# Kernel optimization log

Hardware: AMD Instinct MI355X
Metric: run time of the kernel (lower is better)

## Reference

```python
import jax, jax.numpy as jnp
import numpy as np

INPUT_DIM = 1024
HIDDEN_DIM = 2048
NUM_BLOCKS = 8
BLOCK_SIZE = HIDDEN_DIM // NUM_BLOCKS
BATCH = 2048


def setup_inputs() -> dict:
    key = jax.random.key(0)
    ks = jax.random.split(key, 6)
    # PyTorch GRUCell init: uniform(-1/sqrt(hidden_size), 1/sqrt(hidden_size))
    bound = 1.0 / np.sqrt(BLOCK_SIZE)
    u = lambda k, shape: jax.random.uniform(k, shape, jnp.float32, -bound, bound)
    return {
        "input": jax.random.normal(ks[0], (BATCH, INPUT_DIM), jnp.float32),
        "hidden": jax.random.normal(ks[1], (BATCH, HIDDEN_DIM), jnp.float32),
        # stacked per-block GRUCell params (block-diagonal structure)
        "W_ih": u(ks[2], (NUM_BLOCKS, 3 * BLOCK_SIZE, INPUT_DIM)),
        "W_hh": u(ks[3], (NUM_BLOCKS, 3 * BLOCK_SIZE, BLOCK_SIZE)),
        "b_ih": u(ks[4], (NUM_BLOCKS, 3 * BLOCK_SIZE)),
        "b_hh": u(ks[5], (NUM_BLOCKS, 3 * BLOCK_SIZE)),
    }


def reference(input, hidden, W_ih, W_hh, b_ih, b_hh):
    B = input.shape[0]
    nb, g3, bs = W_hh.shape  # [num_blocks, 3*block_size, block_size]
    hb = hidden.reshape(B, nb, bs)                      # [B, nb, bs]
    # input-to-gate and hidden-to-gate projections, batched over blocks
    gi = jnp.einsum("bi,ngi->bng", input, W_ih) + b_ih  # [B, nb, 3*bs]
    gh = jnp.einsum("bns,ngs->bng", hb, W_hh) + b_hh    # [B, nb, 3*bs]
    i_r, i_z, i_n = jnp.split(gi, 3, axis=-1)
    h_r, h_z, h_n = jnp.split(gh, 3, axis=-1)
    r = jax.nn.sigmoid(i_r + h_r)
    z = jax.nn.sigmoid(i_z + h_z)
    n = jnp.tanh(i_n + r * h_n)
    new_h = (1.0 - z) * n + z * hb                      # [B, nb, bs]
    return new_h.reshape(B, nb * bs)
```

## Files before the change

kernel.cpp:

```cpp
#include <hip/hip_runtime.h>
#include <hip/hip_bf16.h>
#include <type_traits>

#define AS1 __attribute__((address_space(1)))
#define AS3 __attribute__((address_space(3)))

typedef __attribute__((ext_vector_type(4))) float f32x4;
typedef __attribute__((ext_vector_type(8))) short bf16x8;

template <int V> using ic = std::integral_constant<int, V>;

static constexpr int B_   = 2048;
static constexpr int IN_  = 1024;
static constexpr int HID_ = 2048;
static constexpr int NB_  = 8;
static constexpr int BS_  = 256;
static constexpr int G3_  = 768;

__device__ __forceinline__ unsigned short f2bf(float f) {
  unsigned u = __builtin_bit_cast(unsigned, f);
  u = (u + 0x7FFFu + ((u >> 16) & 1u)) >> 16;
  return (unsigned short)u;
}

__global__ void cvt_all(const float* __restrict__ x, const float* __restrict__ h,
                        const float* __restrict__ Wih, const float* __restrict__ Whh,
                        unsigned short* __restrict__ dst) {
  constexpr int c0 = (B_ * IN_) / 4;
  constexpr int c1 = c0 + (B_ * HID_) / 4;
  constexpr int c2 = c1 + (NB_ * G3_ * IN_) / 4;
  constexpr int n4 = c2 + (NB_ * G3_ * BS_) / 4;
  int i = blockIdx.x * blockDim.x + threadIdx.x;
  int stride = gridDim.x * blockDim.x;
  for (; i < n4; i += stride) {
    float4 v;
    if (i < c0)       v = reinterpret_cast<const float4*>(x)[i];
    else if (i < c1)  v = reinterpret_cast<const float4*>(h)[i - c0];
    else if (i < c2)  v = reinterpret_cast<const float4*>(Wih)[i - c1];
    else              v = reinterpret_cast<const float4*>(Whh)[i - c2];
    ushort4 o;
    o.x = f2bf(v.x); o.y = f2bf(v.y); o.z = f2bf(v.z); o.w = f2bf(v.w);
    reinterpret_cast<ushort4*>(dst)[i] = o;
  }
}

__global__ __launch_bounds__(256, 2) void gru_mfma(
    const unsigned short* __restrict__ inb,
    const unsigned short* __restrict__ hidb,
    const unsigned short* __restrict__ wihb,
    const unsigned short* __restrict__ whhb,
    const float* __restrict__ hid_f32,
    const float* __restrict__ b_ih,
    const float* __restrict__ b_hh,
    float* __restrict__ out)
{
  __shared__ __align__(16) char lds[2][40960];

  const int t    = threadIdx.x;
  const int lane = t & 63;
  const int wid  = t >> 6;
  const int wm   = wid >> 1;
  const int wn   = wid & 1;

  const int bid = blockIdx.x;
  const int swz = (bid & 7) * 64 + (bid >> 3);
  const int mt  = swz & 15;
  const int ct  = swz >> 4;
  const int mrow0 = mt * 128;
  const int n     = ct >> 2;
  const int s0    = (ct & 3) * 64;

  int arow[4], acb[4];
#pragma unroll
  for (int p = 0; p < 4; ++p) {
    int op = p * 4096 + t * 16;
    int ol = op ^ (((op >> 7) & 7) << 4);
    arow[p] = ol >> 7; acb[p] = ol & 127;
  }
  int wrowg[6], wsl[6], wcb[6];
#pragma unroll
  for (int p = 0; p < 6; ++p) {
    int op = p * 4096 + t * 16;
    int ol = op ^ (((op >> 7) & 7) << 4);
    int wr = ol >> 7;
    wrowg[p] = wr >> 6;
    wsl[p]   = wr & 63;
    wcb[p]   = ol & 127;
  }

  f32x4 acc[4][4][2] = {};

  auto stage = [&](int buf, int t2, int from, int to) {
    const bool ph1 = t2 < 16;
    const int ks = ph1 ? t2 : (t2 - 16);
    char* base = (char*)lds[buf];
#pragma unroll
    for (int p = 0; p < 10; ++p) {
      if (p < from || p >= to) continue;
      if (p < 4) {
        const char* src = ph1
          ? (const char*)inb  + ((size_t)(mrow0 + arow[p]) * IN_  + ks * 64) * 2 + acb[p]
          : (const char*)hidb + ((size_t)(mrow0 + arow[p]) * HID_ + n * BS_ + ks * 64) * 2 + acb[p];
        __builtin_amdgcn_global_load_lds((const AS1 void*)src,
                                         (AS3 void*)(base + p * 4096 + wid * 1024), 16, 0, 0);
      } else {
        const int q = p - 4;
        int grow = n * G3_ + wrowg[q] * BS_ + s0 + wsl[q];
        const char* src = ph1
          ? (const char*)wihb + ((size_t)grow * IN_ + ks * 64) * 2 + wcb[q]
          : (const char*)whhb + ((size_t)grow * BS_ + ks * 64) * 2 + wcb[q];
        __builtin_amdgcn_global_load_lds((const AS1 void*)src,
                                         (AS3 void*)(base + 16384 + q * 4096 + wid * 1024), 16, 0, 0);
      }
    }
  };

  auto loadA = [&](int buf, bf16x8 (&af)[2][4]) {
#pragma unroll
    for (int ksub = 0; ksub < 2; ++ksub)
#pragma unroll
      for (int mi = 0; mi < 4; ++mi) {
        int ar  = wm * 64 + mi * 16 + (lane & 15);
        int off = ar * 128 + ksub * 64 + ((lane >> 4) * 16);
        off ^= (ar & 7) << 4;
        af[ksub][mi] = *reinterpret_cast<const bf16x8*>((const char*)lds[buf] + off);
      }
  };
  auto loadW = [&](int buf, int g, bf16x8 (&wf)[2][2]) {
#pragma unroll
    for (int ksub = 0; ksub < 2; ++ksub)
#pragma unroll
      for (int ni = 0; ni < 2; ++ni) {
        int wr  = g * 64 + wn * 32 + ni * 16 + (lane & 15);
        int off = wr * 128 + ksub * 64 + ((lane >> 4) * 16);
        off ^= (wr & 7) << 4;
        wf[ksub][ni] = *reinterpret_cast<const bf16x8*>((const char*)lds[buf] + 16384 + off);
      }
  };
  auto mfmaSet = [&](auto setc, bf16x8 (&af)[2][4], bf16x8 (&wf)[2][2]) {
    constexpr int set = decltype(setc)::value;
    __builtin_amdgcn_s_setprio(1);
#pragma unroll
    for (int ksub = 0; ksub < 2; ++ksub)
#pragma unroll
      for (int mi = 0; mi < 4; ++mi)
#pragma unroll
        for (int ni = 0; ni < 2; ++ni)
          acc[set][mi][ni] = __builtin_amdgcn_mfma_f32_16x16x32_bf16(
              af[ksub][mi], wf[ksub][ni], acc[set][mi][ni], 0, 0, 0);
    __builtin_amdgcn_s_setprio(0);
  };

  stage(0, 0, 0, 10);
  stage(1, 1, 0, 8);
  __builtin_amdgcn_sched_barrier(0);
  asm volatile("s_waitcnt vmcnt(8)");
  __builtin_amdgcn_sched_barrier(0);
  __builtin_amdgcn_s_barrier();

#pragma unroll
  for (int tt = 0; tt < 20; ++tt) {
    const int cur = tt & 1, oth = cur ^ 1;
    bf16x8 af[2][4], wf[2][2];

    loadA(cur, af);
    loadW(cur, 0, wf);
    if (tt + 1 < 20) stage(oth, tt + 1, 8, 10);
    __builtin_amdgcn_s_barrier();
    asm volatile("s_waitcnt lgkmcnt(0)");
    __builtin_amdgcn_sched_barrier(0);
    mfmaSet(ic<0>{}, af, wf);
    __builtin_amdgcn_s_barrier();

    loadW(cur, 1, wf);
    if (tt + 2 < 20) stage(cur, tt + 2, 0, 6);
    __builtin_amdgcn_s_barrier();
    asm volatile("s_waitcnt lgkmcnt(0)");
    __builtin_amdgcn_sched_barrier(0);
    mfmaSet(ic<1>{}, af, wf);
    __builtin_amdgcn_s_barrier();

    loadW(cur, 2, wf);
    if (tt + 2 < 20) stage(cur, tt + 2, 6, 8);
    __builtin_amdgcn_sched_barrier(0);
    if (tt <= 17)      asm volatile("s_waitcnt vmcnt(8)");
    else if (tt == 18) asm volatile("s_waitcnt vmcnt(0)");
    __builtin_amdgcn_sched_barrier(0);
    __builtin_amdgcn_s_barrier();
    asm volatile("s_waitcnt lgkmcnt(0)");
    __builtin_amdgcn_sched_barrier(0);
    if (tt < 16) mfmaSet(ic<2>{}, af, wf);
    else         mfmaSet(ic<3>{}, af, wf);
    __builtin_amdgcn_s_barrier();
  }

#pragma unroll
  for (int ni = 0; ni < 2; ++ni) {
    int scol = s0 + wn * 32 + ni * 16 + (lane & 15);
    float br_i = b_ih[n * G3_ + 0 * BS_ + scol];
    float bz_i = b_ih[n * G3_ + 1 * BS_ + scol];
    float bn_i = b_ih[n * G3_ + 2 * BS_ + scol];
    float br_h = b_hh[n * G3_ + 0 * BS_ + scol];
    float bz_h = b_hh[n * G3_ + 1 * BS_ + scol];
    float bn_h = b_hh[n * G3_ + 2 * BS_ + scol];
    int gcol = n * BS_ + scol;
#pragma unroll
    for (int mi = 0; mi < 4; ++mi) {
#pragma unroll
      for (int i = 0; i < 4; ++i) {
        int row = mrow0 + wm * 64 + mi * 16 + (lane >> 4) * 4 + i;
        float hprev = hid_f32[(size_t)row * HID_ + gcol];
        float rr = acc[0][mi][ni][i] + br_i + br_h;
        float zz = acc[1][mi][ni][i] + bz_i + bz_h;
        float r  = 1.f / (1.f + __expf(-rr));
        float z  = 1.f / (1.f + __expf(-zz));
        float ng = tanhf(acc[2][mi][ni][i] + bn_i + r * (acc[3][mi][ni][i] + bn_h));
        out[(size_t)row * HID_ + gcol] = (1.f - z) * ng + z * hprev;
      }
    }
  }
}

__global__ void gru_naive(const float* __restrict__ x, const float* __restrict__ h,
                          const float* __restrict__ Wih, const float* __restrict__ Whh,
                          const float* __restrict__ bih, const float* __restrict__ bhh,
                          float* __restrict__ out) {
  int b = blockIdx.x;
  int n = blockIdx.y;
  int s = threadIdx.x;
  __shared__ float xs[1024];
  __shared__ float hs[256];
  for (int i = threadIdx.x; i < 1024; i += 256) xs[i] = x[(size_t)b * IN_ + i];
  if (threadIdx.x < 256) hs[threadIdx.x] = h[(size_t)b * HID_ + n * BS_ + threadIdx.x];
  __syncthreads();
  float gi[3], gh[3];
  for (int g = 0; g < 3; ++g) {
    const float* w = Wih + ((size_t)(n * G3_ + g * BS_ + s)) * IN_;
    float a = 0.f;
    for (int k = 0; k < IN_; ++k) a += xs[k] * w[k];
    gi[g] = a + bih[n * G3_ + g * BS_ + s];
    const float* w2 = Whh + ((size_t)(n * G3_ + g * BS_ + s)) * BS_;
    float a2 = 0.f;
    for (int k = 0; k < BS_; ++k) a2 += hs[k] * w2[k];
    gh[g] = a2 + bhh[n * G3_ + g * BS_ + s];
  }
  float r = 1.f / (1.f + expf(-(gi[0] + gh[0])));
  float z = 1.f / (1.f + expf(-(gi[1] + gh[1])));
  float ng = tanhf(gi[2] + r * gh[2]);
  out[(size_t)b * HID_ + n * BS_ + s] = (1.f - z) * ng + z * hs[s];
}

extern "C" void kernel_launch(void* const* d_in, const int* in_sizes, int n_in,
                              void* d_out, int out_size, void* d_ws, size_t ws_size,
                              hipStream_t stream) {
  const float* x   = (const float*)d_in[0];
  const float* h   = (const float*)d_in[1];
  const float* Wih = (const float*)d_in[2];
  const float* Whh = (const float*)d_in[3];
  const float* bih = (const float*)d_in[4];
  const float* bhh = (const float*)d_in[5];
  float* out = (float*)d_out;

  const size_t szin  = (size_t)B_ * IN_;
  const size_t szhid = (size_t)B_ * HID_;
  const size_t szwih = (size_t)NB_ * G3_ * IN_;
  const size_t szwhh = (size_t)NB_ * G3_ * BS_;
  const size_t need  = (szin + szhid + szwih + szwhh) * 2;

  if (ws_size >= need) {
    unsigned short* inb  = (unsigned short*)d_ws;
    unsigned short* hidb = inb + szin;
    unsigned short* wihb = hidb + szhid;
    unsigned short* whhb = wihb + szwih;
    cvt_all<<<2048, 256, 0, stream>>>(x, h, Wih, Whh, (unsigned short*)d_ws);
    gru_mfma<<<512, 256, 0, stream>>>(inb, hidb, wihb, whhb, h, bih, bhh, out);
  } else {
    dim3 grid(B_, NB_);
    gru_naive<<<grid, 256, 0, stream>>>(x, h, Wih, Whh, bih, bhh, out);
  }
}
```

Measured before the change: 56.89 us.

## Fuse fp32-to-bf16 conversion into GEMM staging, drop separate convert kernel

Removes the standalone conversion kernel that wrote bf16 copies of inputs and weights to workspace. The GEMM kernel now loads fp32 tiles into registers, converts them to bf16 and writes them to LDS itself, prefetching the next k-step through registers instead of direct global-to-LDS async loads. This saves a launch and a full extra read and write of all operands. In exchange it doubles global read bytes per tile, adds conversion ALU work and register pressure inside the main loop, and replaces the hand-tuned waitcnt/barrier schedule with plain __syncthreads. The naive fallback path is also removed.

After: 58.53 us. 2.9% more time.

```diff
diff --git a/kernel.cpp b/kernel.cpp
--- a/kernel.cpp
+++ b/kernel.cpp
@@ -1,9 +1,6 @@
 #include <hip/hip_runtime.h>
 #include <hip/hip_bf16.h>
 #include <type_traits>
-
-#define AS1 __attribute__((address_space(1)))
-#define AS3 __attribute__((address_space(3)))
 
 typedef __attribute__((ext_vector_type(4))) float f32x4;
 typedef __attribute__((ext_vector_type(8))) short bf16x8;
@@ -23,33 +20,11 @@
   return (unsigned short)u;
 }
 
-__global__ void cvt_all(const float* __restrict__ x, const float* __restrict__ h,
-                        const float* __restrict__ Wih, const float* __restrict__ Whh,
-                        unsigned short* __restrict__ dst) {
-  constexpr int c0 = (B_ * IN_) / 4;
-  constexpr int c1 = c0 + (B_ * HID_) / 4;
-  constexpr int c2 = c1 + (NB_ * G3_ * IN_) / 4;
-  constexpr int n4 = c2 + (NB_ * G3_ * BS_) / 4;
-  int i = blockIdx.x * blockDim.x + threadIdx.x;
-  int stride = gridDim.x * blockDim.x;
-  for (; i < n4; i += stride) {
-    float4 v;
-    if (i < c0)       v = reinterpret_cast<const float4*>(x)[i];
-    else if (i < c1)  v = reinterpret_cast<const float4*>(h)[i - c0];
-    else if (i < c2)  v = reinterpret_cast<const float4*>(Wih)[i - c1];
-    else              v = reinterpret_cast<const float4*>(Whh)[i - c2];
-    ushort4 o;
-    o.x = f2bf(v.x); o.y = f2bf(v.y); o.z = f2bf(v.z); o.w = f2bf(v.w);
-    reinterpret_cast<ushort4*>(dst)[i] = o;
-  }
-}
-
 __global__ __launch_bounds__(256, 2) void gru_mfma(
-    const unsigned short* __restrict__ inb,
-    const unsigned short* __restrict__ hidb,
-    const unsigned short* __restrict__ wihb,
-    const unsigned short* __restrict__ whhb,
-    const float* __restrict__ hid_f32,
+    const float* __restrict__ xf,
+    const float* __restrict__ hf,
+    const float* __restrict__ Wih,
+    const float* __restrict__ Whh,
     const float* __restrict__ b_ih,
     const float* __restrict__ b_hh,
     float* __restrict__ out)
@@ -64,58 +39,74 @@
 
   const int bid = blockIdx.x;
   const int swz = (bid & 7) * 64 + (bid >> 3);
-  const int mt  = swz & 15;
-  const int ct  = swz >> 4;
-  const int mrow0 = mt * 128;
+  const int mrow0 = (swz & 15) * 128;
+  const int ct    = swz >> 4;
   const int n     = ct >> 2;
   const int s0    = (ct & 3) * 64;
 
-  int arow[4], acb[4];
+  int arow[4], acol[4];
 #pragma unroll
   for (int p = 0; p < 4; ++p) {
     int op = p * 4096 + t * 16;
     int ol = op ^ (((op >> 7) & 7) << 4);
-    arow[p] = ol >> 7; acb[p] = ol & 127;
-  }
-  int wrowg[6], wsl[6], wcb[6];
-#pragma unroll
-  for (int p = 0; p < 6; ++p) {
-    int op = p * 4096 + t * 16;
+    arow[p] = ol >> 7;
+    acol[p] = (ol & 127) >> 1;
+  }
+  int wgrow[6], wcol[6];
+#pragma unroll
+  for (int q = 0; q < 6; ++q) {
+    int op = q * 4096 + t * 16;
     int ol = op ^ (((op >> 7) & 7) << 4);
     int wr = ol >> 7;
-    wrowg[p] = wr >> 6;
-    wsl[p]   = wr & 63;
-    wcb[p]   = ol & 127;
+    wgrow[q] = n * G3_ + (wr >> 6) * BS_ + s0 + (wr & 63);
+    wcol[q]  = (ol & 127) >> 1;
   }
 
   f32x4 acc[4][4][2] = {};
-
-  auto stage = [&](int buf, int t2, int from, int to) {
-    const bool ph1 = t2 < 16;
-    const int ks = ph1 ? t2 : (t2 - 16);
-    char* base = (char*)lds[buf];
-#pragma unroll
-    for (int p = 0; p < 10; ++p) {
-      if (p < from || p >= to) continue;
-      if (p < 4) {
-        const char* src = ph1
-          ? (const char*)inb  + ((size_t)(mrow0 + arow[p]) * IN_  + ks * 64) * 2 + acb[p]
-          : (const char*)hidb + ((size_t)(mrow0 + arow[p]) * HID_ + n * BS_ + ks * 64) * 2 + acb[p];
-        __builtin_amdgcn_global_load_lds((const AS1 void*)src,
-                                         (AS3 void*)(base + p * 4096 + wid * 1024), 16, 0, 0);
-      } else {
-        const int q = p - 4;
-        int grow = n * G3_ + wrowg[q] * BS_ + s0 + wsl[q];
-        const char* src = ph1
-          ? (const char*)wihb + ((size_t)grow * IN_ + ks * 64) * 2 + wcb[q]
-          : (const char*)whhb + ((size_t)grow * BS_ + ks * 64) * 2 + wcb[q];
-        __builtin_amdgcn_global_load_lds((const AS1 void*)src,
-                                         (AS3 void*)(base + 16384 + q * 4096 + wid * 1024), 16, 0, 0);
-      }
+  float4 sa[4][2];
+  float4 sw[3][2];
+
+  auto issueA = [&](int t2) {
+#pragma unroll
+    for (int p = 0; p < 4; ++p) {
+      const float* src = (t2 < 16)
+        ? xf + (size_t)(mrow0 + arow[p]) * IN_  + t2 * 64 + acol[p]
+        : hf + (size_t)(mrow0 + arow[p]) * HID_ + n * BS_ + (t2 - 16) * 64 + acol[p];
+      sa[p][0] = *reinterpret_cast<const float4*>(src);
+      sa[p][1] = *reinterpret_cast<const float4*>(src + 4);
     }
   };
-
-  auto loadA = [&](int buf, bf16x8 (&af)[2][4]) {
+  auto issueW = [&](int t2, int q0) {
+#pragma unroll
+    for (int j = 0; j < 3; ++j) {
+      const int q = q0 + j;
+      const float* src = (t2 < 16)
+        ? Wih + (size_t)wgrow[q] * IN_ + t2 * 64 + wcol[q]
+        : Whh + (size_t)wgrow[q] * BS_ + (t2 - 16) * 64 + wcol[q];
+      sw[j][0] = *reinterpret_cast<const float4*>(src);
+      sw[j][1] = *reinterpret_cast<const float4*>(src + 4);
+    }
+  };
+  auto pack = [](const float4 (&v)[2]) {
+    union { bf16x8 b; unsigned short s[8]; } u;
+    u.s[0] = f2bf(v[0].x); u.s[1] = f2bf(v[0].y);
+    u.s[2] = f2bf(v[0].z); u.s[3] = f2bf(v[0].w);
+    u.s[4] = f2bf(v[1].x); u.s[5] = f2bf(v[1].y);
+    u.s[6] = f2bf(v[1].z); u.s[7] = f2bf(v[1].w);
+    return u.b;
+  };
+  auto writeA = [&](char* buf) {
+#pragma unroll
+    for (int p = 0; p < 4; ++p)
+      *reinterpret_cast<bf16x8*>(buf + p * 4096 + t * 16) = pack(sa[p]);
+  };
+  auto writeW = [&](char* buf, int q0) {
+#pragma unroll
+    for (int j = 0; j < 3; ++j)
+      *reinterpret_cast<bf16x8*>(buf + 16384 + (q0 + j) * 4096 + t * 16) = pack(sw[j]);
+  };
+
+  auto loadA = [&](const char* buf, bf16x8 (&af)[2][4]) {
 #pragma unroll
     for (int ksub = 0; ksub < 2; ++ksub)
 #pragma unroll
@@ -123,10 +114,10 @@
         int ar  = wm * 64 + mi * 16 + (lane & 15);
         int off = ar * 128 + ksub * 64 + ((lane >> 4) * 16);
         off ^= (ar & 7) << 4;
-        af[ksub][mi] = *reinterpret_cast<const bf16x8*>((const char*)lds[buf] + off);
+        af[ksub][mi] = *reinterpret_cast<const bf16x8*>(buf + off);
       }
   };
-  auto loadW = [&](int buf, int g, bf16x8 (&wf)[2][2]) {
+  auto loadW = [&](const char* buf, int g, bf16x8 (&wf)[2][2]) {
 #pragma unroll
     for (int ksub = 0; ksub < 2; ++ksub)
 #pragma unroll
@@ -134,12 +125,11 @@
         int wr  = g * 64 + wn * 32 + ni * 16 + (lane & 15);
         int off = wr * 128 + ksub * 64 + ((lane >> 4) * 16);
         off ^= (wr & 7) << 4;
-        wf[ksub][ni] = *reinterpret_cast<const bf16x8*>((const char*)lds[buf] + 16384 + off);
+        wf[ksub][ni] = *reinterpret_cast<const bf16x8*>(buf + 16384 + off);
       }
   };
   auto mfmaSet = [&](auto setc, bf16x8 (&af)[2][4], bf16x8 (&wf)[2][2]) {
     constexpr int set = decltype(setc)::value;
-    __builtin_amdgcn_s_setprio(1);
 #pragma unroll
     for (int ksub = 0; ksub < 2; ++ksub)
 #pragma unroll
@@ -148,50 +138,35 @@
         for (int ni = 0; ni < 2; ++ni)
           acc[set][mi][ni] = __builtin_amdgcn_mfma_f32_16x16x32_bf16(
               af[ksub][mi], wf[ksub][ni], acc[set][mi][ni], 0, 0, 0);
-    __builtin_amdgcn_s_setprio(0);
-  };
-
-  stage(0, 0, 0, 10);
-  stage(1, 1, 0, 8);
-  __builtin_amdgcn_sched_barrier(0);
-  asm volatile("s_waitcnt vmcnt(8)");
-  __builtin_amdgcn_sched_barrier(0);
-  __builtin_amdgcn_s_barrier();
+  };
+
+  issueA(0);
+  issueW(0, 0);
+  writeA((char*)lds[0]);
+  writeW((char*)lds[0], 0);
+  issueW(0, 3);
+  writeW((char*)lds[0], 3);
+  __syncthreads();
 
 #pragma unroll
   for (int tt = 0; tt < 20; ++tt) {
-    const int cur = tt & 1, oth = cur ^ 1;
+    char* cur = (char*)lds[tt & 1];
+    char* oth = (char*)lds[(tt & 1) ^ 1];
     bf16x8 af[2][4], wf[2][2];
 
+    if (tt < 19) issueA(tt + 1);
     loadA(cur, af);
     loadW(cur, 0, wf);
-    if (tt + 1 < 20) stage(oth, tt + 1, 8, 10);
-    __builtin_amdgcn_s_barrier();
-    asm volatile("s_waitcnt lgkmcnt(0)");
-    __builtin_amdgcn_sched_barrier(0);
     mfmaSet(ic<0>{}, af, wf);
-    __builtin_amdgcn_s_barrier();
-
+    if (tt < 19) { writeA(oth); issueW(tt + 1, 0); }
     loadW(cur, 1, wf);
-    if (tt + 2 < 20) stage(cur, tt + 2, 0, 6);
-    __builtin_amdgcn_s_barrier();
-    asm volatile("s_waitcnt lgkmcnt(0)");
-    __builtin_amdgcn_sched_barrier(0);
     mfmaSet(ic<1>{}, af, wf);
-    __builtin_amdgcn_s_barrier();
-
+    if (tt < 19) { writeW(oth, 0); issueW(tt + 1, 3); }
     loadW(cur, 2, wf);
-    if (tt + 2 < 20) stage(cur, tt + 2, 6, 8);
-    __builtin_amdgcn_sched_barrier(0);
-    if (tt <= 17)      asm volatile("s_waitcnt vmcnt(8)");
-    else if (tt == 18) asm volatile("s_waitcnt vmcnt(0)");
-    __builtin_amdgcn_sched_barrier(0);
-    __builtin_amdgcn_s_barrier();
-    asm volatile("s_waitcnt lgkmcnt(0)");
-    __builtin_amdgcn_sched_barrier(0);
     if (tt < 16) mfmaSet(ic<2>{}, af, wf);
     else         mfmaSet(ic<3>{}, af, wf);
-    __builtin_amdgcn_s_barrier();
+    if (tt < 19) writeW(oth, 3);
+    __syncthreads();
   }
 
 #pragma unroll
@@ -209,7 +184,7 @@
 #pragma unroll
       for (int i = 0; i < 4; ++i) {
         int row = mrow0 + wm * 64 + mi * 16 + (lane >> 4) * 4 + i;
-        float hprev = hid_f32[(size_t)row * HID_ + gcol];
+        float hprev = hf[(size_t)row * HID_ + gcol];
         float rr = acc[0][mi][ni][i] + br_i + br_h;
         float zz = acc[1][mi][ni][i] + bz_i + bz_h;
         float r  = 1.f / (1.f + __expf(-rr));
@@ -219,35 +194,6 @@
       }
     }
   }
-}
-
-__global__ void gru_naive(const float* __restrict__ x, const float* __restrict__ h,
-                          const float* __restrict__ Wih, const float* __restrict__ Whh,
-                          const float* __restrict__ bih, const float* __restrict__ bhh,
-                          float* __restrict__ out) {
-  int b = blockIdx.x;
-  int n = blockIdx.y;
-  int s = threadIdx.x;
-  __shared__ float xs[1024];
-  __shared__ float hs[256];
-  for (int i = threadIdx.x; i < 1024; i += 256) xs[i] = x[(size_t)b * IN_ + i];
-  if (threadIdx.x < 256) hs[threadIdx.x] = h[(size_t)b * HID_ + n * BS_ + threadIdx.x];
-  __syncthreads();
-  float gi[3], gh[3];
-  for (int g = 0; g < 3; ++g) {
-    const float* w = Wih + ((size_t)(n * G3_ + g * BS_ + s)) * IN_;
-    float a = 0.f;
-    for (int k = 0; k < IN_; ++k) a += xs[k] * w[k];
-    gi[g] = a + bih[n * G3_ + g * BS_ + s];
-    const float* w2 = Whh + ((size_t)(n * G3_ + g * BS_ + s)) * BS_;
-    float a2 = 0.f;
-    for (int k = 0; k < BS_; ++k) a2 += hs[k] * w2[k];
-    gh[g] = a2 + bhh[n * G3_ + g * BS_ + s];
-  }
-  float r = 1.f / (1.f + expf(-(gi[0] + gh[0])));
-  float z = 1.f / (1.f + expf(-(gi[1] + gh[1])));
-  float ng = tanhf(gi[2] + r * gh[2]);
-  out[(size_t)b * HID_ + n * BS_ + s] = (1.f - z) * ng + z * hs[s];
 }
 
 extern "C" void kernel_launch(void* const* d_in, const int* in_sizes, int n_in,
@@ -260,22 +206,7 @@
   const float* bih = (const float*)d_in[4];
   const float* bhh = (const float*)d_in[5];
   float* out = (float*)d_out;
-
-  const size_t szin  = (size_t)B_ * IN_;
-  const size_t szhid = (size_t)B_ * HID_;
-  const size_t szwih = (size_t)NB_ * G3_ * IN_;
-  const size_t szwhh = (size_t)NB_ * G3_ * BS_;
-  const size_t need  = (szin + szhid + szwih + szwhh) * 2;
-
-  if (ws_size >= need) {
-    unsigned short* inb  = (unsigned short*)d_ws;
-    unsigned short* hidb = inb + szin;
-    unsigned short* wihb = hidb + szhid;
-    unsigned short* whhb = wihb + szwih;
-    cvt_all<<<2048, 256, 0, stream>>>(x, h, Wih, Whh, (unsigned short*)d_ws);
-    gru_mfma<<<512, 256, 0, stream>>>(inb, hidb, wihb, whhb, h, bih, bhh, out);
-  } else {
-    dim3 grid(B_, NB_);
-    gru_naive<<<grid, 256, 0, stream>>>(x, h, Wih, Whh, bih, bhh, out);
-  }
+  (void)d_ws; (void)ws_size;
+
+  gru_mfma<<<512, 256, 0, stream>>>(x, h, Wih, Whh, bih, bhh, out);
 }
```

## Widen GRU MFMA tile to 128x128 columns with 512-thread blocks

Applied to the files above, without the earlier changes.

Doubles the per-block output-column tile from 64 to 128 hidden units, using 8 waves (2x4) and 512 threads per block. The grid halves to 256 blocks, so each A tile (input/hidden rows) is loaded once for twice the weight columns. This cuts A-side global traffic and the number of blocks. Staging is split into separate A and W loaders, with a reordered wait placement, and the bias loads are hoisted ahead of the main loop. The trade-off is a larger 128KB LDS footprint and fewer blocks, which may reduce occupancy and leave some of the 256 CUs idle.

Measured after the change: 58.93 us. +3.6%, slower.

```diff
diff --git a/kernel.cpp b/kernel.cpp
--- a/kernel.cpp
+++ b/kernel.cpp
@@ -44,7 +44,7 @@
   }
 }
 
-__global__ __launch_bounds__(256, 2) void gru_mfma(
+__global__ __launch_bounds__(512, 2) void gru_mfma(
     const unsigned short* __restrict__ inb,
     const unsigned short* __restrict__ hidb,
     const unsigned short* __restrict__ wihb,
@@ -54,64 +54,83 @@
     const float* __restrict__ b_hh,
     float* __restrict__ out)
 {
-  __shared__ __align__(16) char lds[2][40960];
+  __shared__ __align__(16) char lds[2][65536];
 
   const int t    = threadIdx.x;
   const int lane = t & 63;
   const int wid  = t >> 6;
-  const int wm   = wid >> 1;
-  const int wn   = wid & 1;
+  const int wm   = wid >> 2;
+  const int wn   = wid & 3;
 
   const int bid = blockIdx.x;
-  const int swz = (bid & 7) * 64 + (bid >> 3);
-  const int mt  = swz & 15;
-  const int ct  = swz >> 4;
-  const int mrow0 = mt * 128;
-  const int n     = ct >> 2;
-  const int s0    = (ct & 3) * 64;
-
-  int arow[4], acb[4];
-#pragma unroll
-  for (int p = 0; p < 4; ++p) {
-    int op = p * 4096 + t * 16;
+  const int swz = (bid & 7) * 32 + (bid >> 3);
+  const int mrow0 = (swz & 15) * 128;
+  const int ct2   = swz >> 4;
+  const int n     = ct2 >> 1;
+  const int s0    = (ct2 & 1) * 128;
+
+  int arow[2], acb[2];
+#pragma unroll
+  for (int p = 0; p < 2; ++p) {
+    int op = p * 8192 + t * 16;
     int ol = op ^ (((op >> 7) & 7) << 4);
-    arow[p] = ol >> 7; acb[p] = ol & 127;
-  }
-  int wrowg[6], wsl[6], wcb[6];
-#pragma unroll
-  for (int p = 0; p < 6; ++p) {
-    int op = p * 4096 + t * 16;
+    arow[p] = ol >> 7;
+    acb[p]  = ol & 127;
+  }
+  int wgr[6], wcb[6];
+#pragma unroll
+  for (int q = 0; q < 6; ++q) {
+    int op = q * 8192 + t * 16;
     int ol = op ^ (((op >> 7) & 7) << 4);
     int wr = ol >> 7;
-    wrowg[p] = wr >> 6;
-    wsl[p]   = wr & 63;
-    wcb[p]   = ol & 127;
-  }
+    wgr[q] = n * G3_ + (wr >> 7) * BS_ + s0 + (wr & 127);
+    wcb[q] = ol & 127;
+  }
+
+  float brz[2], bni[2], bnh[2];
+#pragma unroll
+  for (int ni = 0; ni < 2; ++ni) {
+    int scol = s0 + wn * 32 + ni * 16 + (lane & 15);
+    brz[ni] = b_ih[n * G3_ + 0 * BS_ + scol] + b_hh[n * G3_ + 0 * BS_ + scol];
+    bni[ni] = b_ih[n * G3_ + 2 * BS_ + scol];
+    bnh[ni] = b_hh[n * G3_ + 2 * BS_ + scol];
+  }
+  float bz[2];
+#pragma unroll
+  for (int ni = 0; ni < 2; ++ni) {
+    int scol = s0 + wn * 32 + ni * 16 + (lane & 15);
+    bz[ni] = b_ih[n * G3_ + 1 * BS_ + scol] + b_hh[n * G3_ + 1 * BS_ + scol];
+  }
+  asm volatile("s_waitcnt vmcnt(0)");
+  __builtin_amdgcn_sched_barrier(0);
 
   f32x4 acc[4][4][2] = {};
 
-  auto stage = [&](int buf, int t2, int from, int to) {
+  auto stageA = [&](int buf, int t2) {
     const bool ph1 = t2 < 16;
     const int ks = ph1 ? t2 : (t2 - 16);
     char* base = (char*)lds[buf];
 #pragma unroll
-    for (int p = 0; p < 10; ++p) {
-      if (p < from || p >= to) continue;
-      if (p < 4) {
-        const char* src = ph1
-          ? (const char*)inb  + ((size_t)(mrow0 + arow[p]) * IN_  + ks * 64) * 2 + acb[p]
-          : (const char*)hidb + ((size_t)(mrow0 + arow[p]) * HID_ + n * BS_ + ks * 64) * 2 + acb[p];
-        __builtin_amdgcn_global_load_lds((const AS1 void*)src,
-                                         (AS3 void*)(base + p * 4096 + wid * 1024), 16, 0, 0);
-      } else {
-        const int q = p - 4;
-        int grow = n * G3_ + wrowg[q] * BS_ + s0 + wsl[q];
-        const char* src = ph1
-          ? (const char*)wihb + ((size_t)grow * IN_ + ks * 64) * 2 + wcb[q]
-          : (const char*)whhb + ((size_t)grow * BS_ + ks * 64) * 2 + wcb[q];
-        __builtin_amdgcn_global_load_lds((const AS1 void*)src,
-                                         (AS3 void*)(base + 16384 + q * 4096 + wid * 1024), 16, 0, 0);
-      }
+    for (int p = 0; p < 2; ++p) {
+      const char* src = ph1
+        ? (const char*)inb  + ((size_t)(mrow0 + arow[p]) * IN_  + ks * 64) * 2 + acb[p]
+        : (const char*)hidb + ((size_t)(mrow0 + arow[p]) * HID_ + n * BS_ + ks * 64) * 2 + acb[p];
+      __builtin_amdgcn_global_load_lds((const AS1 void*)src,
+                                       (AS3 void*)(base + p * 8192 + wid * 1024), 16, 0, 0);
+    }
+  };
+  auto stageW = [&](int buf, int t2, int g) {
+    const bool ph1 = t2 < 16;
+    const int ks = ph1 ? t2 : (t2 - 16);
+    char* base = (char*)lds[buf] + 16384;
+#pragma unroll
+    for (int j = 0; j < 2; ++j) {
+      const int q = 2 * g + j;
+      const char* src = ph1
+        ? (const char*)wihb + ((size_t)wgr[q] * IN_ + ks * 64) * 2 + wcb[q]
+        : (const char*)whhb + ((size_t)wgr[q] * BS_ + ks * 64) * 2 + wcb[q];
+      __builtin_amdgcn_global_load_lds((const AS1 void*)src,
+                                       (AS3 void*)(base + q * 8192 + wid * 1024), 16, 0, 0);
     }
   };
 
@@ -131,13 +150,13 @@
     for (int ksub = 0; ksub < 2; ++ksub)
 #pragma unroll
       for (int ni = 0; ni < 2; ++ni) {
-        int wr  = g * 64 + wn * 32 + ni * 16 + (lane & 15);
+        int wr  = g * 128 + wn * 32 + ni * 16 + (lane & 15);
         int off = wr * 128 + ksub * 64 + ((lane >> 4) * 16);
         off ^= (wr & 7) << 4;
         wf[ksub][ni] = *reinterpret_cast<const bf16x8*>((const char*)lds[buf] + 16384 + off);
       }
   };
-  auto mfmaSet = [&](auto setc, bf16x8 (&af)[2][4], bf16x8 (&wf)[2][2]) {
+  auto mfma16 = [&](auto setc, bf16x8 (&af)[2][4], bf16x8 (&wf)[2][2]) {
     constexpr int set = decltype(setc)::value;
     __builtin_amdgcn_s_setprio(1);
 #pragma unroll
@@ -151,10 +170,9 @@
     __builtin_amdgcn_s_setprio(0);
   };
 
-  stage(0, 0, 0, 10);
-  stage(1, 1, 0, 8);
-  __builtin_amdgcn_sched_barrier(0);
-  asm volatile("s_waitcnt vmcnt(8)");
+  stageA(0, 0); stageW(0, 0, 0); stageW(0, 0, 1); stageW(0, 0, 2);
+  stageA(1, 1); stageW(1, 1, 0); stageW(1, 1, 1);
+  asm volatile("s_waitcnt vmcnt(6)");
   __builtin_amdgcn_sched_barrier(0);
   __builtin_amdgcn_s_barrier();
 
@@ -165,44 +183,37 @@
 
     loadA(cur, af);
     loadW(cur, 0, wf);
-    if (tt + 1 < 20) stage(oth, tt + 1, 8, 10);
+    if (tt + 1 < 20) stageW(oth, tt + 1, 2);
     __builtin_amdgcn_s_barrier();
     asm volatile("s_waitcnt lgkmcnt(0)");
     __builtin_amdgcn_sched_barrier(0);
-    mfmaSet(ic<0>{}, af, wf);
+    mfma16(ic<0>{}, af, wf);
     __builtin_amdgcn_s_barrier();
 
     loadW(cur, 1, wf);
-    if (tt + 2 < 20) stage(cur, tt + 2, 0, 6);
+    if (tt + 2 < 20) { stageA(cur, tt + 2); stageW(cur, tt + 2, 0); }
     __builtin_amdgcn_s_barrier();
     asm volatile("s_waitcnt lgkmcnt(0)");
     __builtin_amdgcn_sched_barrier(0);
-    mfmaSet(ic<1>{}, af, wf);
+    mfma16(ic<1>{}, af, wf);
     __builtin_amdgcn_s_barrier();
 
     loadW(cur, 2, wf);
-    if (tt + 2 < 20) stage(cur, tt + 2, 6, 8);
-    __builtin_amdgcn_sched_barrier(0);
-    if (tt <= 17)      asm volatile("s_waitcnt vmcnt(8)");
+    if (tt + 2 < 20) stageW(cur, tt + 2, 1);
+    __builtin_amdgcn_s_barrier();
+    asm volatile("s_waitcnt lgkmcnt(0)");
+    __builtin_amdgcn_sched_barrier(0);
+    if (tt < 16) mfma16(ic<2>{}, af, wf);
+    else         mfma16(ic<3>{}, af, wf);
+    if (tt < 18)       asm volatile("s_waitcnt vmcnt(6)");
     else if (tt == 18) asm volatile("s_waitcnt vmcnt(0)");
     __builtin_amdgcn_sched_barrier(0);
-    __builtin_amdgcn_s_barrier();
-    asm volatile("s_waitcnt lgkmcnt(0)");
-    __builtin_amdgcn_sched_barrier(0);
-    if (tt < 16) mfmaSet(ic<2>{}, af, wf);
-    else         mfmaSet(ic<3>{}, af, wf);
     __builtin_amdgcn_s_barrier();
   }
 
 #pragma unroll
   for (int ni = 0; ni < 2; ++ni) {
     int scol = s0 + wn * 32 + ni * 16 + (lane & 15);
-    float br_i = b_ih[n * G3_ + 0 * BS_ + scol];
-    float bz_i = b_ih[n * G3_ + 1 * BS_ + scol];
-    float bn_i = b_ih[n * G3_ + 2 * BS_ + scol];
-    float br_h = b_hh[n * G3_ + 0 * BS_ + scol];
-    float bz_h = b_hh[n * G3_ + 1 * BS_ + scol];
-    float bn_h = b_hh[n * G3_ + 2 * BS_ + scol];
     int gcol = n * BS_ + scol;
 #pragma unroll
     for (int mi = 0; mi < 4; ++mi) {
@@ -210,11 +221,11 @@
       for (int i = 0; i < 4; ++i) {
         int row = mrow0 + wm * 64 + mi * 16 + (lane >> 4) * 4 + i;
         float hprev = hid_f32[(size_t)row * HID_ + gcol];
-        float rr = acc[0][mi][ni][i] + br_i + br_h;
-        float zz = acc[1][mi][ni][i] + bz_i + bz_h;
+        float rr = acc[0][mi][ni][i] + brz[ni];
+        float zz = acc[1][mi][ni][i] + bz[ni];
         float r  = 1.f / (1.f + __expf(-rr));
         float z  = 1.f / (1.f + __expf(-zz));
-        float ng = tanhf(acc[2][mi][ni][i] + bn_i + r * (acc[3][mi][ni][i] + bn_h));
+        float ng = tanhf(acc[2][mi][ni][i] + bni[ni] + r * (acc[3][mi][ni][i] + bnh[ni]));
         out[(size_t)row * HID_ + gcol] = (1.f - z) * ng + z * hprev;
       }
     }
@@ -273,7 +284,7 @@
     unsigned short* wihb = hidb + szhid;
     unsigned short* whhb = wihb + szwih;
     cvt_all<<<2048, 256, 0, stream>>>(x, h, Wih, Whh, (unsigned short*)d_ws);
-    gru_mfma<<<512, 256, 0, stream>>>(inb, hidb, wihb, whhb, h, bih, bhh, out);
+    gru_mfma<<<256, 512, 0, stream>>>(inb, hidb, wihb, whhb, h, bih, bhh, out);
   } else {
     dim3 grid(B_, NB_);
     gru_naive<<<grid, 256, 0, stream>>>(x, h, Wih, Whh, bih, bhh, out);
```
